# Kernel tuning notes

Measured on AMD Instinct MI355X. Metric: run time of the kernel, lower is better.

The kernel has to match this reference:

```python
import jax, jax.numpy as jnp
import numpy as np

B, T, D = 2, 2048, 1024
H, DH, CTX = 16, 64, 2048
EPS = 1e-6

def setup_inputs() -> dict:
    key = jax.random.key(0)
    ks = jax.random.split(key, 8)
    s = lambda d: 1.0 / np.sqrt(d)
    return {
        'x':       jax.random.normal(ks[0], (B, T, D), jnp.float32),
        'w_norm1': jnp.ones((D,), jnp.float32),
        'w_qkv':   jax.random.normal(ks[1], (3 * D, D), jnp.float32) * s(D),
        'w_proj':  jax.random.normal(ks[2], (D, D), jnp.float32) * s(D),
        'w_norm2': jnp.ones((D,), jnp.float32),
        'w_gate':  jax.random.normal(ks[3], (4 * D, D), jnp.float32) * s(D),
        'w_up':    jax.random.normal(ks[4], (4 * D, D), jnp.float32) * s(D),
        'w_down':  jax.random.normal(ks[5], (D, 4 * D), jnp.float32) * s(4 * D),
        'step':    0,
    }

def _rmsnorm(x, w):
    return x * jax.lax.rsqrt(jnp.mean(x * x, axis=-1, keepdims=True) + EPS) * w

def reference(x, w_norm1, w_qkv, w_proj, w_norm2, w_gate, w_up, w_down, step):
    # Prefill path (kv_cache is None, step == 0): full causal attention over T tokens.
    b, t, d = x.shape
    scale = 1.0 / np.sqrt(DH)
    h = _rmsnorm(x, w_norm1)
    qkv = (h @ w_qkv.T).reshape(b, t, 3, H, DH).transpose(2, 0, 3, 1, 4)  # [3,B,H,T,Dh]
    q, k, v = qkv[0], qkv[1], qkv[2]
    att = jnp.einsum('bhqd,bhkd->bhqk', q, k) * scale           # [B,H,T,T]
    causal = jnp.tril(jnp.ones((t, t), bool))
    att = jnp.where(causal, att, jnp.float32(-jnp.inf))
    att = jax.nn.softmax(att, axis=-1)
    out = jnp.einsum('bhqk,bhkd->bhqd', att, v)                 # [B,H,T,Dh]
    out = out.transpose(0, 2, 1, 3).reshape(b, t, d)
    x = x + out @ w_proj.T
    h2 = _rmsnorm(x, w_norm2)
    x = x + (jax.nn.silu(h2 @ w_gate.T) * (h2 @ w_up.T)) @ w_down.T
    # Append-only KV cache, zero-padded to ctx length as in the torch module.
    k_cache = jnp.zeros((b, H, CTX, DH), x.dtype).at[:, :, :t].set(k)
    v_cache = jnp.zeros((b, H, CTX, DH), x.dtype).at[:, :, :t].set(v)
    return (x, k_cache, v_cache)
```

## Files before the change

kernel.cpp:

```cpp
#include <hip/hip_runtime.h>
#include <hip/hip_bf16.h>
#include <cstdint>
#include <cstddef>


using bf16x8 = __attribute__((ext_vector_type(8))) __bf16;
using f32x4  = __attribute__((ext_vector_type(4))) float;

#define VMCNT(n) asm volatile("s_waitcnt vmcnt(" #n ")" ::: "memory")
#define LGKM0()  do { asm volatile("s_waitcnt lgkmcnt(0)" ::: "memory"); \
                      __builtin_amdgcn_sched_barrier(0); } while (0)
#define BARF()   do { asm volatile("" ::: "memory"); __builtin_amdgcn_s_barrier(); \
                      asm volatile("" ::: "memory"); } while (0)

__device__ __forceinline__ short f2b(float f) {
  uint32_t u = __builtin_bit_cast(uint32_t, f);
  uint32_t r = (u + 0x7FFFu + ((u >> 16) & 1u)) >> 16;
  return (short)r;
}
__device__ __forceinline__ float b2f(short s) {
  uint32_t u = ((uint32_t)(uint16_t)s) << 16;
  return __builtin_bit_cast(float, u);
}
__device__ __forceinline__ uint32_t pack2(float a, float b) {
  return (__builtin_bit_cast(uint32_t, a) >> 16) |
         (__builtin_bit_cast(uint32_t, b) & 0xFFFF0000u);
}

__device__ __forceinline__ void gload16(const short* g, short* l) {
  __builtin_amdgcn_global_load_lds(
      (const __attribute__((address_space(1))) void*)g,
      (__attribute__((address_space(3))) void*)l, 16, 0, 0);
}

template<int ROWS>
__device__ __forceinline__ void stage_swz(const short* __restrict__ g, int ldg,
                                          short* lds, int tid) {
#pragma unroll
  for (int jj = 0; jj < ROWS / 32; ++jj) {
    int row = jj * 32 + (tid >> 3);
    int seg = tid & 7;
    gload16(g + (size_t)row * ldg + ((seg ^ (row & 7)) << 3),
            lds + row * 64 + (seg << 3));
  }
}

__device__ __forceinline__ void stage_round512(const short* __restrict__ g, int ldg,
                                               short* lds, int tid, int rbase) {
  int row = rbase + (tid >> 3);
  int seg = tid & 7;
  gload16(g + (size_t)row * ldg + ((seg ^ (row & 7)) << 3),
          lds + row * 64 + (seg << 3));
}

__device__ __forceinline__ bf16x8 frag64(const short* lds, int row, int seg) {
  return *(const bf16x8*)(lds + row * 64 + ((seg ^ (row & 7)) << 3));
}

__device__ __forceinline__ f32x4 mma16(bf16x8 a, bf16x8 b, f32x4 c) {
  return __builtin_amdgcn_mfma_f32_16x16x32_bf16(a, b, c, 0, 0, 0);
}

__global__ void k_cvt_all(const float* __restrict__ wqkv, short* __restrict__ oqkv,
                          const float* __restrict__ wproj, short* __restrict__ oproj,
                          const float* __restrict__ wgate, short* __restrict__ ogate,
                          const float* __restrict__ wup, short* __restrict__ oup,
                          const float* __restrict__ wdown, short* __restrict__ odown) {
  int bid = blockIdx.x;
  const float* src;
  short* dst;
  int off;
  if (bid < 3072)       { src = wqkv;  dst = oqkv;  off = bid; }
  else if (bid < 4096)  { src = wproj; dst = oproj; off = bid - 3072; }
  else if (bid < 8192)  { src = wgate; dst = ogate; off = bid - 4096; }
  else if (bid < 12288) { src = wup;   dst = oup;   off = bid - 8192; }
  else                  { src = wdown; dst = odown; off = bid - 12288; }
  int i = off * 256 + threadIdx.x;
  float4 v = ((const float4*)src)[i];
  ((short4*)dst)[i] = make_short4(f2b(v.x), f2b(v.y), f2b(v.z), f2b(v.w));
}

__global__ void k_rms(const float* __restrict__ x, const float* __restrict__ w,
                      short* __restrict__ out) {
  int row = blockIdx.x;
  int tid = threadIdx.x;
  float4 v = *(const float4*)(x + (size_t)row * 1024 + tid * 4);
  float ss = v.x * v.x + v.y * v.y + v.z * v.z + v.w * v.w;
#pragma unroll
  for (int o = 1; o < 64; o <<= 1) ss += __shfl_xor(ss, o);
  __shared__ float sred[4];
  int wid = tid >> 6, lane = tid & 63;
  if (lane == 0) sred[wid] = ss;
  __syncthreads();
  float tot = sred[0] + sred[1] + sred[2] + sred[3];
  float r = rsqrtf(tot * (1.0f / 1024.0f) + 1e-6f);
  float4 wv = *(const float4*)(w + tid * 4);
  short4 o = make_short4(f2b(v.x * r * wv.x), f2b(v.y * r * wv.y),
                         f2b(v.z * r * wv.z), f2b(v.w * r * wv.w));
  *(short4*)(out + (size_t)row * 1024 + tid * 4) = o;
}

__global__ __launch_bounds__(512) void k_qkv(
    const short* __restrict__ A, const short* __restrict__ W,
    short* __restrict__ q_b, short* __restrict__ k_b, short* __restrict__ vT_b,
    float* __restrict__ kc, float* __restrict__ vc) {
  const int K = 1024, nk = 16;
  __shared__ short As[2][128 * 64];
  __shared__ short Bq[2][128 * 64];
  __shared__ short Bk[2][128 * 64];
  __shared__ short Bv[2][128 * 64];
  int tid = threadIdx.x;
  int bid = blockIdx.x;
  int swz = (bid & 7) * 32 + (bid >> 3);
  int bx = swz & 7, by = swz >> 3;
  int m0 = by * 128, n0 = bx * 128;
  int w = tid >> 6, l = tid & 63;
  int wr = w >> 2, wc = w & 3;
  int lr = l & 15, lseg = l >> 4;
  f32x4 aq[4][2] = {}, ak[4][2] = {}, av[4][2] = {};
  const short* Ab = A + (size_t)m0 * K;
  const short* Qb = W + (size_t)n0 * K;
  const short* Kb = W + (size_t)(1024 + n0) * K;
  const short* Vb = W + (size_t)(2048 + n0) * K;

  stage_round512(Ab, K, &As[0][0], tid, 0);
  stage_round512(Ab, K, &As[0][0], tid, 64);
  stage_round512(Qb, K, &Bq[0][0], tid, 0);
  stage_round512(Qb, K, &Bq[0][0], tid, 64);
  stage_round512(Kb, K, &Bk[0][0], tid, 0);
  stage_round512(Kb, K, &Bk[0][0], tid, 64);
  stage_round512(Vb, K, &Bv[0][0], tid, 0);
  stage_round512(Vb, K, &Bv[0][0], tid, 64);
  stage_round512(Ab + 64, K, &As[1][0], tid, 0);
  stage_round512(Ab + 64, K, &As[1][0], tid, 64);

  bf16x8 a[4][2], b[2][2];
#pragma unroll 2
  for (int t = 0; t < nk; ++t) {
    short* Sa = &As[t & 1][0];
    short* Sq = &Bq[t & 1][0];
    short* Sk = &Bk[t & 1][0];
    short* Sv = &Bv[t & 1][0];
    short* SqN = &Bq[(t + 1) & 1][0];
    short* SkN = &Bk[(t + 1) & 1][0];
    short* SvN = &Bv[(t + 1) & 1][0];
    const short* Ag2 = Ab + (size_t)(t + 2) * 64;
    const short* Qg1 = Qb + (size_t)(t + 1) * 64;
    const short* Kg1 = Kb + (size_t)(t + 1) * 64;
    const short* Vg1 = Vb + (size_t)(t + 1) * 64;
    bool pf1 = (t + 1 < nk), pf2 = (t + 2 < nk);

    VMCNT(2);
    BARF();

#pragma unroll
    for (int i = 0; i < 4; ++i)
#pragma unroll
      for (int kk = 0; kk < 2; ++kk)
        a[i][kk] = frag64(Sa, wr * 64 + i * 16 + lr, kk * 4 + lseg);
#pragma unroll
    for (int j = 0; j < 2; ++j)
#pragma unroll
      for (int kk = 0; kk < 2; ++kk)
        b[j][kk] = frag64(Sq, wc * 32 + j * 16 + lr, kk * 4 + lseg);
    if (pf1) {
      stage_round512(Qg1, K, SqN, tid, 0);
      stage_round512(Qg1, K, SqN, tid, 64);
      stage_round512(Kg1, K, SkN, tid, 0);
      stage_round512(Kg1, K, SkN, tid, 64);
    }
    BARF();
    LGKM0();
    __builtin_amdgcn_s_setprio(1);
#pragma unroll
    for (int i = 0; i < 4; ++i)
#pragma unroll
      for (int j = 0; j < 2; ++j) {
        aq[i][j] = mma16(a[i][0], b[j][0], aq[i][j]);
        aq[i][j] = mma16(a[i][1], b[j][1], aq[i][j]);
      }
    __builtin_amdgcn_s_setprio(0);

#pragma unroll
    for (int j = 0; j < 2; ++j)
#pragma unroll
      for (int kk = 0; kk < 2; ++kk)
        b[j][kk] = frag64(Sk, wc * 32 + j * 16 + lr, kk * 4 + lseg);
    if (pf1) {
      stage_round512(Vg1, K, SvN, tid, 0);
      stage_round512(Vg1, K, SvN, tid, 64);
    }
    BARF();
    LGKM0();
    __builtin_amdgcn_s_setprio(1);
#pragma unroll
    for (int i = 0; i < 4; ++i)
#pragma unroll
      for (int j = 0; j < 2; ++j) {
        ak[i][j] = mma16(a[i][0], b[j][0], ak[i][j]);
        ak[i][j] = mma16(a[i][1], b[j][1], ak[i][j]);
      }
    __builtin_amdgcn_s_setprio(0);

#pragma unroll
    for (int j = 0; j < 2; ++j)
#pragma unroll
      for (int kk = 0; kk < 2; ++kk)
        b[j][kk] = frag64(Sv, wc * 32 + j * 16 + lr, kk * 4 + lseg);
    if (pf2) {
      stage_round512(Ag2, K, Sa, tid, 0);
      stage_round512(Ag2, K, Sa, tid, 64);
    }
    BARF();
    LGKM0();
    __builtin_amdgcn_s_setprio(1);
#pragma unroll
    for (int i = 0; i < 4; ++i)
#pragma unroll
      for (int j = 0; j < 2; ++j) {
        av[i][j] = mma16(a[i][0], b[j][0], av[i][j]);
        av[i][j] = mma16(a[i][1], b[j][1], av[i][j]);
      }
    __builtin_amdgcn_s_setprio(0);
  }

#pragma unroll
  for (int i = 0; i < 4; ++i) {
#pragma unroll
    for (int j = 0; j < 2; ++j) {
#pragma unroll
      for (int r = 0; r < 4; ++r) {
        int m = m0 + wr * 64 + i * 16 + lseg * 4 + r;
        int n = n0 + wc * 32 + j * 16 + lr;
        int hh = n >> 6, dh = n & 63;
        int b_ = m >> 11, tt = m & 2047;
        int bh = b_ * 16 + hh;
        size_t idx = ((size_t)bh * 2048 + tt) * 64 + dh;
        q_b[idx] = f2b(aq[i][j][r]);
        float fk = ak[i][j][r];
        k_b[idx] = f2b(fk);
        kc[idx] = fk;
        float fv = av[i][j][r];
        vT_b[((size_t)bh * 64 + dh) * 2048 + tt] = f2b(fv);
        vc[idx] = fv;
      }
    }
  }
}

__global__ __launch_bounds__(512) void k_mlp(
    const short* __restrict__ A, const short* __restrict__ Wg,
    const short* __restrict__ Wu, short* __restrict__ outb) {
  const int K = 1024, N = 4096, nk = 16;
  __shared__ short As[2][256 * 64];
  __shared__ short Bg[2][128 * 64];
  __shared__ short Bu[2][128 * 64];
  int tid = threadIdx.x;
  int bid = blockIdx.x;
  int xcd = bid & 7, idx = bid >> 3;
  int bx = xcd * 4 + (idx & 3);
  int by = idx >> 2;
  int m0 = by * 256, n0 = bx * 128;
  int w = tid >> 6, l = tid & 63;
  int wr = w >> 2, wc = w & 3;
  int lr = l & 15, lseg = l >> 4;
  f32x4 aG[2][4][2] = {}, aU[2][4][2] = {};
  const short* Ab = A + (size_t)m0 * K;
  const short* Gb = Wg + (size_t)n0 * K;
  const short* Ub = Wu + (size_t)n0 * K;

  stage_round512(Ab, K, &As[0][0], tid, 0);
  stage_round512(Ab, K, &As[0][0], tid, 64);
  stage_round512(Ab, K, &As[0][0], tid, 128);
  stage_round512(Ab, K, &As[0][0], tid, 192);
  stage_round512(Gb, K, &Bg[0][0], tid, 0);
  stage_round512(Gb, K, &Bg[0][0], tid, 64);
  stage_round512(Ub, K, &Bu[0][0], tid, 0);
  stage_round512(Ub, K, &Bu[0][0], tid, 64);
  stage_round512(Ab + 64, K, &As[1][0], tid, 0);
  stage_round512(Ab + 64, K, &As[1][0], tid, 64);
  stage_round512(Ab + 64, K, &As[1][0], tid, 128);
  stage_round512(Ab + 64, K, &As[1][0], tid, 192);

  bf16x8 a0[4][2], a1[4][2], bg[2][2], bu[2][2];
#pragma unroll 2
  for (int t = 0; t < nk; ++t) {
    short* Sa  = &As[t & 1][0];
    short* Sg  = &Bg[t & 1][0];
    short* Su  = &Bu[t & 1][0];
    short* SgN = &Bg[(t + 1) & 1][0];
    short* SuN = &Bu[(t + 1) & 1][0];
    const short* Ag2 = Ab + (size_t)(t + 2) * 64;
    const short* Gg1 = Gb + (size_t)(t + 1) * 64;
    const short* Ug1 = Ub + (size_t)(t + 1) * 64;
    bool pf1 = (t + 1 < nk), pf2 = (t + 2 < nk);

    VMCNT(4);
    BARF();

#pragma unroll
    for (int i = 0; i < 4; ++i)
#pragma unroll
      for (int kk = 0; kk < 2; ++kk)
        a0[i][kk] = frag64(Sa, wr * 128 + i * 16 + lr, kk * 4 + lseg);
#pragma unroll
    for (int j = 0; j < 2; ++j)
#pragma unroll
      for (int kk = 0; kk < 2; ++kk)
        bg[j][kk] = frag64(Sg, wc * 32 + j * 16 + lr, kk * 4 + lseg);
    if (pf1) {
      stage_round512(Gg1, K, SgN, tid, 0);
      stage_round512(Gg1, K, SgN, tid, 64);
      stage_round512(Ug1, K, SuN, tid, 0);
      stage_round512(Ug1, K, SuN, tid, 64);
    }
    BARF();
    LGKM0();
    __builtin_amdgcn_s_setprio(1);
#pragma unroll
    for (int i = 0; i < 4; ++i)
#pragma unroll
      for (int j = 0; j < 2; ++j) {
        aG[0][i][j] = mma16(a0[i][0], bg[j][0], aG[0][i][j]);
        aG[0][i][j] = mma16(a0[i][1], bg[j][1], aG[0][i][j]);
      }
    __builtin_amdgcn_s_setprio(0);

#pragma unroll
    for (int j = 0; j < 2; ++j)
#pragma unroll
      for (int kk = 0; kk < 2; ++kk)
        bu[j][kk] = frag64(Su, wc * 32 + j * 16 + lr, kk * 4 + lseg);
    if (pf2) {
      stage_round512(Ag2, K, Sa, tid, 0);
      stage_round512(Ag2, K, Sa, tid, 128);
    }
    BARF();
    LGKM0();
    __builtin_amdgcn_s_setprio(1);
#pragma unroll
    for (int i = 0; i < 4; ++i)
#pragma unroll
      for (int j = 0; j < 2; ++j) {
        aU[0][i][j] = mma16(a0[i][0], bu[j][0], aU[0][i][j]);
        aU[0][i][j] = mma16(a0[i][1], bu[j][1], aU[0][i][j]);
      }
    __builtin_amdgcn_s_setprio(0);

#pragma unroll
    for (int i = 0; i < 4; ++i)
#pragma unroll
      for (int kk = 0; kk < 2; ++kk)
        a1[i][kk] = frag64(Sa, wr * 128 + 64 + i * 16 + lr, kk * 4 + lseg);
    BARF();
    LGKM0();
    __builtin_amdgcn_s_setprio(1);
#pragma unroll
    for (int i = 0; i < 4; ++i)
#pragma unroll
      for (int j = 0; j < 2; ++j) {
        aG[1][i][j] = mma16(a1[i][0], bg[j][0], aG[1][i][j]);
        aG[1][i][j] = mma16(a1[i][1], bg[j][1], aG[1][i][j]);
      }
    __builtin_amdgcn_s_setprio(0);

    if (pf2) {
      stage_round512(Ag2, K, Sa, tid, 64);
      stage_round512(Ag2, K, Sa, tid, 192);
    }
    BARF();
    __builtin_amdgcn_s_setprio(1);
#pragma unroll
    for (int i = 0; i < 4; ++i)
#pragma unroll
      for (int j = 0; j < 2; ++j) {
        aU[1][i][j] = mma16(a1[i][0], bu[j][0], aU[1][i][j]);
        aU[1][i][j] = mma16(a1[i][1], bu[j][1], aU[1][i][j]);
      }
    __builtin_amdgcn_s_setprio(0);
  }

#pragma unroll
  for (int qm = 0; qm < 2; ++qm) {
#pragma unroll
    for (int i = 0; i < 4; ++i) {
#pragma unroll
      for (int j = 0; j < 2; ++j) {
#pragma unroll
        for (int r = 0; r < 4; ++r) {
          int m = m0 + wr * 128 + qm * 64 + i * 16 + lseg * 4 + r;
          int n = n0 + wc * 32 + j * 16 + lr;
          float g = aG[qm][i][j][r];
          float u = aU[qm][i][j][r];
          float s = g / (1.0f + __expf(-g));
          outb[(size_t)m * N + n] = f2b(s * u);
        }
      }
    }
  }
}

__global__ __launch_bounds__(256, 2) void k_gemm_skinny(
    const short* __restrict__ A, const short* __restrict__ Bw,
    int M, int N, int K, int gx,
    const float* __restrict__ res, float* __restrict__ outf) {
  __shared__ short As[3][128 * 64];
  __shared__ short Bs[3][64 * 64];
  int tid = threadIdx.x;
  int nwg = gridDim.x, bid = blockIdx.x;
  int swz = (bid & 7) * (nwg >> 3) + (bid >> 3);
  int bx = swz % gx, by = swz / gx;
  int m0 = by * 128, n0 = bx * 64;
  int w = tid >> 6, l = tid & 63;
  int wr = w >> 1, wc = w & 1;
  int lr = l & 15, lseg = l >> 4;
  f32x4 acc[4][2] = {};
  int nk = K >> 6;
  const short* Ab = A + (size_t)m0 * K;
  const short* Bb = Bw + (size_t)n0 * K;

  stage_swz<128>(Ab, K, &As[0][0], tid);
  stage_swz<64>(Bb, K, &Bs[0][0], tid);
  stage_swz<128>(Ab + 64, K, &As[1][0], tid);
  stage_swz<64>(Bb + 64, K, &Bs[1][0], tid);

#pragma unroll 1
  for (int u = 0; u < nk; ++u) {
    VMCNT(6);
    BARF();
    if (u + 2 < nk) {
      int sl = (u + 2) % 3;
      stage_swz<128>(Ab + (u + 2) * 64, K, &As[sl][0], tid);
      stage_swz<64>(Bb + (u + 2) * 64, K, &Bs[sl][0], tid);
    }
    const short* Asl = &As[u % 3][0];
    const short* Bsl = &Bs[u % 3][0];
    bf16x8 ar[4][2], br[2][2];
#pragma unroll
    for (int i = 0; i < 4; ++i)
#pragma unroll
      for (int kk = 0; kk < 2; ++kk)
        ar[i][kk] = frag64(Asl, wr * 64 + i * 16 + lr, kk * 4 + lseg);
#pragma unroll
    for (int j = 0; j < 2; ++j)
#pragma unroll
      for (int kk = 0; kk < 2; ++kk)
        br[j][kk] = frag64(Bsl, wc * 32 + j * 16 + lr, kk * 4 + lseg);
    LGKM0();
    __builtin_amdgcn_s_setprio(1);
#pragma unroll
    for (int i = 0; i < 4; ++i)
#pragma unroll
      for (int j = 0; j < 2; ++j) {
        acc[i][j] = mma16(ar[i][0], br[j][0], acc[i][j]);
        acc[i][j] = mma16(ar[i][1], br[j][1], acc[i][j]);
      }
    __builtin_amdgcn_s_setprio(0);
  }

#pragma unroll
  for (int i = 0; i < 4; ++i) {
#pragma unroll
    for (int j = 0; j < 2; ++j) {
#pragma unroll
      for (int r = 0; r < 4; ++r) {
        int m = m0 + wr * 64 + i * 16 + (l >> 4) * 4 + r;
        int n = n0 + wc * 32 + j * 16 + lr;
        outf[(size_t)m * N + n] = acc[i][j][r] + res[(size_t)m * N + n];
      }
    }
  }
}

template<int NC>
__device__ __forceinline__ void attn_tile(
    const short* __restrict__ Ksl, const short* __restrict__ Vsl,
    short* __restrict__ pw,
    const bf16x8 (&qf)[2][2], f32x4 (&acc)[2][4],
    float (&mrow)[2], float (&dden)[2],
    int kv0, int qb0, int qb1, bool band0, bool band1,
    int lr, int g) {
  bf16x8 kf[4][2], vb[2][4];
#pragma unroll
  for (int i = 0; i < 4; ++i)
#pragma unroll
    for (int kk = 0; kk < 2; ++kk)
      kf[i][kk] = frag64(Ksl, i * 16 + lr, kk * 4 + g);
#pragma unroll
  for (int kk = 0; kk < 2; ++kk)
#pragma unroll
    for (int jf = 0; jf < 4; ++jf)
      vb[kk][jf] = frag64(Vsl, jf * 16 + lr, kk * 4 + g);

  f32x4 st[NC][4];
#pragma unroll
  for (int c = 0; c < NC; ++c) {
    int cc = (NC == 2) ? c : 1;
#pragma unroll
    for (int i = 0; i < 4; ++i) {
      f32x4 z = {};
      z = mma16(kf[i][0], qf[cc][0], z);
      z = mma16(kf[i][1], qf[cc][1], z);
      st[c][i] = z;
    }
  }

  const float SC = 0.125f * 1.44269504f;
  float p[NC][16], pm[NC], corr[NC];
#pragma unroll
  for (int c = 0; c < NC; ++c) {
    int cc = (NC == 2) ? c : 1;
    bool band = (cc == 0) ? band0 : band1;
    int qgc = ((cc == 0) ? qb0 : qb1) + lr;
    float m_ = -INFINITY;
#pragma unroll
    for (int i = 0; i < 4; ++i)
#pragma unroll
      for (int r = 0; r < 4; ++r) {
        float v = st[c][i][r] * SC;
        if (band) {
          int key = kv0 + i * 16 + g * 4 + r;
          if (key > qgc) v = -INFINITY;
        }
        p[c][i * 4 + r] = v;
        m_ = fmaxf(m_, v);
      }
    pm[c] = m_;
  }
#pragma unroll
  for (int c = 0; c < NC; ++c) pm[c] = fmaxf(pm[c], __shfl_xor(pm[c], 16));
#pragma unroll
  for (int c = 0; c < NC; ++c) pm[c] = fmaxf(pm[c], __shfl_xor(pm[c], 32));
  float dsum[NC];
#pragma unroll
  for (int c = 0; c < NC; ++c) {
    int cc = (NC == 2) ? c : 1;
    float nm = fmaxf(mrow[cc], pm[c]);
    corr[c] = exp2f(mrow[cc] - nm);
    mrow[cc] = nm;
    float ds_ = 0.0f;
#pragma unroll
    for (int kx = 0; kx < 16; ++kx) {
      float pv = exp2f(p[c][kx] - nm);
      p[c][kx] = pv;
      ds_ += pv;
    }
    dsum[c] = ds_;
  }
#pragma unroll
  for (int c = 0; c < NC; ++c) dsum[c] += __shfl_xor(dsum[c], 16);
#pragma unroll
  for (int c = 0; c < NC; ++c) dsum[c] += __shfl_xor(dsum[c], 32);
#pragma unroll
  for (int c = 0; c < NC; ++c) {
    int cc = (NC == 2) ? c : 1;
    dden[cc] = dden[cc] * corr[c] + dsum[c];
  }

#pragma unroll
  for (int c = 0; c < NC; ++c) {
    int cc = (NC == 2) ? c : 1;
#pragma unroll
    for (int r = 0; r < 4; ++r) {
      float cr = __shfl(corr[c], g * 4 + r);
#pragma unroll
      for (int jf = 0; jf < 4; ++jf) acc[cc][jf][r] *= cr;
    }
    int prow = cc * 16 + lr;
#pragma unroll
    for (int i = 0; i < 4; ++i) {
      uint2 pk;
      pk.x = pack2(p[c][i * 4 + 0], p[c][i * 4 + 1]);
      pk.y = pack2(p[c][i * 4 + 2], p[c][i * 4 + 3]);
      int seg = (i * 2 + (g >> 1)) ^ (prow & 7);
      *(uint2*)(pw + prow * 64 + seg * 8 + (g & 1) * 4) = pk;
    }
  }

#pragma unroll
  for (int c = 0; c < NC; ++c) {
    int cc = (NC == 2) ? c : 1;
    int prow = cc * 16 + lr;
#pragma unroll
    for (int kk = 0; kk < 2; ++kk) {
      bf16x8 pa = *(const bf16x8*)(pw + prow * 64 + (((kk * 4 + g) ^ (prow & 7)) << 3));
#pragma unroll
      for (int jf = 0; jf < 4; ++jf)
        acc[cc][jf] = mma16(pa, vb[kk][jf], acc[cc][jf]);
    }
  }
}

__global__ __launch_bounds__(256, 2) void k_attn(const short* __restrict__ q_b,
                                                 const short* __restrict__ k_b,
                                                 const short* __restrict__ vT_b,
                                                 short* __restrict__ o_b) {
  __shared__ short Ks[3][64 * 64];
  __shared__ short VTs[3][64 * 64];
  __shared__ short Ps[4][32 * 64];
  int tid = threadIdx.x;
  int w = tid >> 6, l = tid & 63;
  int lr = l & 15, g = l >> 4;
  int ib = blockIdx.x, bh = blockIdx.y;
  int qlo = ib, qhi = 31 - ib;
  int qb0 = qlo * 64 + w * 16;
  int qb1 = qhi * 64 + w * 16;

  bf16x8 qf[2][2];
  const short* Qg = q_b + (size_t)bh * 2048 * 64;
#pragma unroll
  for (int kk = 0; kk < 2; ++kk) {
    qf[0][kk] = *(const bf16x8*)(Qg + (size_t)(qb0 + lr) * 64 + kk * 32 + g * 8);
    qf[1][kk] = *(const bf16x8*)(Qg + (size_t)(qb1 + lr) * 64 + kk * 32 + g * 8);
  }

  f32x4 acc[2][4] = {};
  float mrow[2] = {-INFINITY, -INFINITY};
  float dden[2] = {0.0f, 0.0f};
  int nt = qhi + 1;
  const short* Kg = k_b + (size_t)bh * 2048 * 64;
  const short* Vg = vT_b + (size_t)bh * 64 * 2048;
  short* pw = &Ps[w][0];

  stage_swz<64>(Kg, 64, &Ks[0][0], tid);
  stage_swz<64>(Vg, 2048, &VTs[0][0], tid);
  stage_swz<64>(Kg + 64 * 64, 64, &Ks[1][0], tid);
  stage_swz<64>(Vg + 64, 2048, &VTs[1][0], tid);

#pragma unroll 1
  for (int kt = 0; kt <= qlo; ++kt) {
    VMCNT(4);
    BARF();
    if (kt + 2 < nt) {
      int sl = (kt + 2) % 3;
      stage_swz<64>(Kg + (size_t)(kt + 2) * 64 * 64, 64, &Ks[sl][0], tid);
      stage_swz<64>(Vg + (kt + 2) * 64, 2048, &VTs[sl][0], tid);
    }
    int s = kt % 3;
    attn_tile<2>(&Ks[s][0], &VTs[s][0], pw, qf, acc, mrow, dden,
                 kt * 64, qb0, qb1, kt == qlo, false, lr, g);
  }
#pragma unroll 1
  for (int kt = qlo + 1; kt < nt; ++kt) {
    VMCNT(4);
    BARF();
    if (kt + 2 < nt) {
      int sl = (kt + 2) % 3;
      stage_swz<64>(Kg + (size_t)(kt + 2) * 64 * 64, 64, &Ks[sl][0], tid);
      stage_swz<64>(Vg + (kt + 2) * 64, 2048, &VTs[sl][0], tid);
    }
    int s = kt % 3;
    attn_tile<1>(&Ks[s][0], &VTs[s][0], pw, qf, acc, mrow, dden,
                 kt * 64, qb0, qb1, false, kt == qhi, lr, g);
  }

  int hh = bh & 15, b_ = bh >> 4;
#pragma unroll
  for (int c = 0; c < 2; ++c) {
    int qbc = (c == 0) ? qb0 : qb1;
#pragma unroll
    for (int r = 0; r < 4; ++r) {
      float dq = __shfl(dden[c], g * 4 + r);
      float inv = 1.0f / dq;
      int mg = qbc + g * 4 + r;
      size_t rowoff = ((size_t)b_ * 2048 + mg) * 1024 + hh * 64;
#pragma unroll
      for (int jf = 0; jf < 4; ++jf)
        o_b[rowoff + jf * 16 + lr] = f2b(acc[c][jf][r] * inv);
    }
  }
}

extern "C" void kernel_launch(void* const* d_in, const int* in_sizes, int n_in,
                              void* d_out, int out_size, void* d_ws, size_t ws_size,
                              hipStream_t stream) {
  const float* x     = (const float*)d_in[0];
  const float* wn1   = (const float*)d_in[1];
  const float* wqkv  = (const float*)d_in[2];
  const float* wproj = (const float*)d_in[3];
  const float* wn2   = (const float*)d_in[4];
  const float* wgate = (const float*)d_in[5];
  const float* wup   = (const float*)d_in[6];
  const float* wdown = (const float*)d_in[7];
  float* out = (float*)d_out;
  char* ws = (char*)d_ws;

  short* wqkv_b  = (short*)(ws + 0);
  short* wproj_b = (short*)(ws + 6291456);
  short* wgate_b = (short*)(ws + 8388608);
  short* wup_b   = (short*)(ws + 16777216);
  short* wdown_b = (short*)(ws + 25165824);
  short* h_b     = (short*)(ws + 33554432);
  short* q_b     = (short*)(ws + 41943040);
  short* k_b     = (short*)(ws + 50331648);
  short* vT_b    = (short*)(ws + 58720256);
  short* ao_b    = (short*)(ws + 67108864);
  short* act_b   = q_b;
  float* x1 = out;
  float* kc = out + 4194304;
  float* vc = out + 8388608;

  k_cvt_all<<<16384, 256, 0, stream>>>(wqkv, wqkv_b, wproj, wproj_b,
                                       wgate, wgate_b, wup, wup_b, wdown, wdown_b);

  k_rms<<<4096, 256, 0, stream>>>(x, wn1, h_b);

  k_qkv<<<256, 512, 0, stream>>>(h_b, wqkv_b, q_b, k_b, vT_b, kc, vc);

  k_attn<<<dim3(16, 32), 256, 0, stream>>>(q_b, k_b, vT_b, ao_b);

  k_gemm_skinny<<<512, 256, 0, stream>>>(ao_b, wproj_b, 4096, 1024, 1024, 16,
                                         x, x1);

  k_rms<<<4096, 256, 0, stream>>>(x1, wn2, h_b);

  k_mlp<<<512, 512, 0, stream>>>(h_b, wgate_b, wup_b, act_b);

  k_gemm_skinny<<<512, 256, 0, stream>>>(act_b, wdown_b, 4096, 1024, 4096, 16,
                                         x1, out);
}
```

Baseline: 275.8 us.

## Replace down-projection GEMM with split-K 256x128 tiled kernel plus reduction pass

The down projection (K=4096) now runs in a new 512-thread kernel with 256x128 output tiles, double-buffered LDS staging and a split-K of two, so the grid has 256 workgroups. Each K half writes bf16 partial sums into reused workspace (the gate/up weight buffers), and a separate elementwise kernel adds both partials to the residual. The larger tiles raise data reuse per block, and split-K keeps enough blocks to fill the GPU. The cost is an extra launch and extra global traffic for the partials, plus rounding the partial sums to bf16 before accumulation.

```diff
diff --git a/kernel.cpp b/kernel.cpp
--- a/kernel.cpp
+++ b/kernel.cpp
@@ -400,6 +400,133 @@
   }
 }
 
+__global__ __launch_bounds__(512) void k_down(
+    const short* __restrict__ A, const short* __restrict__ Bw,
+    short* __restrict__ pc0, short* __restrict__ pc1) {
+  const int K = 4096, nk = 32;
+  __shared__ short As[2][256 * 64];
+  __shared__ short Bs[2][128 * 64];
+  int tid = threadIdx.x;
+  int bid = blockIdx.x;
+  int xcd = bid & 7, idx = bid >> 3;
+  int ks = idx & 1;
+  int by = idx >> 1;
+  int bx = xcd;
+  int m0 = by * 256, n0 = bx * 128;
+  int w = tid >> 6, l = tid & 63;
+  int wr = w >> 2, wc = w & 3;
+  int lr = l & 15, lseg = l >> 4;
+  f32x4 acc[2][4][2] = {};
+  const short* Ab = A + (size_t)m0 * K + ks * 2048;
+  const short* Bb = Bw + (size_t)n0 * K + ks * 2048;
+  short* pc = ks ? pc1 : pc0;
+
+  stage_round512(Ab, K, &As[0][0], tid, 0);
+  stage_round512(Ab, K, &As[0][0], tid, 64);
+  stage_round512(Ab, K, &As[0][0], tid, 128);
+  stage_round512(Ab, K, &As[0][0], tid, 192);
+  stage_round512(Bb, K, &Bs[0][0], tid, 0);
+  stage_round512(Bb, K, &Bs[0][0], tid, 64);
+  stage_round512(Ab + 64, K, &As[1][0], tid, 0);
+  stage_round512(Ab + 64, K, &As[1][0], tid, 128);
+  stage_round512(Bb + 64, K, &Bs[1][0], tid, 0);
+  stage_round512(Bb + 64, K, &Bs[1][0], tid, 64);
+
+  bf16x8 a0[4][2], a1[4][2], b[2][2];
+#pragma unroll 2
+  for (int t = 0; t < nk; ++t) {
+    int s = t & 1;
+    short* Sa = &As[s][0];
+    short* Sb = &Bs[s][0];
+    short* SaN = &As[s ^ 1][0];
+    const short* Ag1 = Ab + (size_t)(t + 1) * 64;
+    const short* Ag2 = Ab + (size_t)(t + 2) * 64;
+    const short* Bg2 = Bb + (size_t)(t + 2) * 64;
+    bool pf1 = (t + 1 < nk), pf2 = (t + 2 < nk);
+
+    VMCNT(4);
+    BARF();
+
+#pragma unroll
+    for (int i = 0; i < 4; ++i)
+#pragma unroll
+      for (int kk = 0; kk < 2; ++kk)
+        a0[i][kk] = frag64(Sa, wr * 128 + i * 16 + lr, kk * 4 + lseg);
+#pragma unroll
+    for (int j = 0; j < 2; ++j)
+#pragma unroll
+      for (int kk = 0; kk < 2; ++kk)
+        b[j][kk] = frag64(Sb, wc * 32 + j * 16 + lr, kk * 4 + lseg);
+    if (pf1) {
+      stage_round512(Ag1, K, SaN, tid, 64);
+      stage_round512(Ag1, K, SaN, tid, 192);
+    }
+    BARF();
+    LGKM0();
+    __builtin_amdgcn_s_setprio(1);
+#pragma unroll
+    for (int i = 0; i < 4; ++i)
+#pragma unroll
+      for (int j = 0; j < 2; ++j) {
+        acc[0][i][j] = mma16(a0[i][0], b[j][0], acc[0][i][j]);
+        acc[0][i][j] = mma16(a0[i][1], b[j][1], acc[0][i][j]);
+      }
+    __builtin_amdgcn_s_setprio(0);
+
+#pragma unroll
+    for (int i = 0; i < 4; ++i)
+#pragma unroll
+      for (int kk = 0; kk < 2; ++kk)
+        a1[i][kk] = frag64(Sa, wr * 128 + 64 + i * 16 + lr, kk * 4 + lseg);
+    BARF();
+    if (pf2) {
+      stage_round512(Ag2, K, Sa, tid, 0);
+      stage_round512(Ag2, K, Sa, tid, 128);
+      stage_round512(Bg2, K, Sb, tid, 0);
+      stage_round512(Bg2, K, Sb, tid, 64);
+    }
+    LGKM0();
+    __builtin_amdgcn_s_setprio(1);
+#pragma unroll
+    for (int i = 0; i < 4; ++i)
+#pragma unroll
+      for (int j = 0; j < 2; ++j) {
+        acc[1][i][j] = mma16(a1[i][0], b[j][0], acc[1][i][j]);
+        acc[1][i][j] = mma16(a1[i][1], b[j][1], acc[1][i][j]);
+      }
+    __builtin_amdgcn_s_setprio(0);
+  }
+
+#pragma unroll
+  for (int qm = 0; qm < 2; ++qm) {
+#pragma unroll
+    for (int i = 0; i < 4; ++i) {
+#pragma unroll
+      for (int j = 0; j < 2; ++j) {
+#pragma unroll
+        for (int r = 0; r < 4; ++r) {
+          int m = m0 + wr * 128 + qm * 64 + i * 16 + lseg * 4 + r;
+          int n = n0 + wc * 32 + j * 16 + lr;
+          pc[(size_t)m * 1024 + n] = f2b(acc[qm][i][j][r]);
+        }
+      }
+    }
+  }
+}
+
+__global__ void k_fin(float* __restrict__ out, const short* __restrict__ pc0,
+                      const short* __restrict__ pc1) {
+  int i = blockIdx.x * 256 + threadIdx.x;
+  float4 v = ((const float4*)out)[i];
+  short4 p0 = ((const short4*)pc0)[i];
+  short4 p1 = ((const short4*)pc1)[i];
+  v.x += b2f(p0.x) + b2f(p1.x);
+  v.y += b2f(p0.y) + b2f(p1.y);
+  v.z += b2f(p0.z) + b2f(p1.z);
+  v.w += b2f(p0.w) + b2f(p1.w);
+  ((float4*)out)[i] = v;
+}
+
 __global__ __launch_bounds__(256, 2) void k_gemm_skinny(
     const short* __restrict__ A, const short* __restrict__ Bw,
     int M, int N, int K, int gx,
@@ -696,6 +823,8 @@
   short* vT_b    = (short*)(ws + 58720256);
   short* ao_b    = (short*)(ws + 67108864);
   short* act_b   = q_b;
+  short* pc0     = wgate_b;
+  short* pc1     = wup_b;
   float* x1 = out;
   float* kc = out + 4194304;
   float* vc = out + 8388608;
@@ -716,6 +845,6 @@
 
   k_mlp<<<512, 512, 0, stream>>>(h_b, wgate_b, wup_b, act_b);
 
-  k_gemm_skinny<<<512, 256, 0, stream>>>(act_b, wdown_b, 4096, 1024, 4096, 16,
-                                         x1, out);
-}
+  k_down<<<256, 512, 0, stream>>>(act_b, wdown_b, pc0, pc1);
+  k_fin<<<4096, 256, 0, stream>>>(out, pc0, pc1);
+}
```

Result: faster. 270.0 us (-2.1%).
